# Kernel optimization log

Measured on AMD Instinct MI355X. Metric: run time of the kernel, lower is better.

The kernel has to match this reference:

```python
import jax, jax.numpy as jnp
import numpy as np

D_MODEL = 1024
NUM_HEADS = 16
HEAD_DIM = D_MODEL // NUM_HEADS
ROPE_BASE = 10000.0


def _rope_cos_sin(seq_len, head_dim, dtype):
    # inv_freq over half the head dim (standard 1D RoPE)
    inv_freq = 1.0 / (ROPE_BASE ** (jnp.arange(0, head_dim, 2, dtype=jnp.float32) / head_dim))
    ang = jnp.arange(seq_len, dtype=jnp.float32)[:, None] * inv_freq[None, :]  # [S, hd/2]
    cos = jnp.concatenate([jnp.cos(ang), jnp.cos(ang)], axis=-1).astype(dtype)  # [S, hd]
    sin = jnp.concatenate([jnp.sin(ang), jnp.sin(ang)], axis=-1).astype(dtype)
    return cos, sin


def _rotate_half(t):
    t1, t2 = jnp.split(t, 2, axis=-1)
    return jnp.concatenate([-t2, t1], axis=-1)


def _apply_rope(t, cos, sin):
    # t: [B, H, S, hd]; cos/sin: [S, hd]
    return t * cos[None, None, :, :] + _rotate_half(t) * sin[None, None, :, :]


def setup_inputs() -> dict:
    key = jax.random.key(0)
    k1, k2, k3 = jax.random.split(key, 3)
    B, S = 2, 2048
    x = jax.random.normal(k1, (B, S, D_MODEL), dtype=jnp.float32)
    w_qkv = jax.random.normal(k2, (D_MODEL, 3 * D_MODEL), dtype=jnp.float32) * (D_MODEL ** -0.5)
    w_proj = jax.random.normal(k3, (D_MODEL, D_MODEL), dtype=jnp.float32) * (D_MODEL ** -0.5)
    b_proj = jnp.zeros((D_MODEL,), dtype=jnp.float32)
    return {"x": x, "w_qkv": w_qkv, "w_proj": w_proj, "b_proj": b_proj, "causal": 1}


def reference(x, w_qkv, w_proj, b_proj, causal):
    B, S, D = x.shape
    scale = HEAD_DIM ** -0.5
    qkv = x @ w_qkv  # [B, S, 3D]
    q, k, v = jnp.split(qkv, 3, axis=-1)

    def to_heads(t):
        return t.reshape(B, S, NUM_HEADS, HEAD_DIM).transpose(0, 2, 1, 3)  # [B,H,S,hd]

    q, k, v = to_heads(q), to_heads(k), to_heads(v)

    cos, sin = _rope_cos_sin(S, HEAD_DIM, x.dtype)
    q = _apply_rope(q, cos, sin)
    k = _apply_rope(k, cos, sin)

    attn = jnp.einsum('bhqd,bhkd->bhqk', q, k) * scale  # [B,H,S,S]
    if causal:
        causal_mask = jnp.triu(jnp.ones((S, S), dtype=bool), k=1)
        attn = jnp.where(causal_mask[None, None, :, :], jnp.float32(-jnp.inf).astype(attn.dtype), attn)
    attn = jax.nn.softmax(attn, axis=-1)
    out = jnp.einsum('bhqk,bhkd->bhqd', attn, v)  # [B,H,S,hd]
    out = out.transpose(0, 2, 1, 3).reshape(B, S, D)
    return out @ w_proj + b_proj
```

## Files before the change

### kernel.cpp

```cpp
#include <hip/hip_runtime.h>
#include <stdint.h>
#include <math.h>

#define B_   2
#define S_   2048
#define D_   1024
#define H_   16
#define HD_  64
#define M_   (B_*S_)
#define N3_  (3*D_)

typedef __bf16 bf16;
typedef __bf16 bf16x2 __attribute__((ext_vector_type(2)));
typedef __bf16 bf16x4v __attribute__((ext_vector_type(4)));
typedef __bf16 bf16x8 __attribute__((ext_vector_type(8)));
typedef float  f32x4 __attribute__((ext_vector_type(4)));
typedef float  f32x16 __attribute__((ext_vector_type(16)));

__device__ __forceinline__ void gload_lds16(const void* g, void* l) {
  __builtin_amdgcn_global_load_lds(
      (__attribute__((address_space(1))) const unsigned int*)g,
      (__attribute__((address_space(3))) unsigned int*)l, 16, 0, 0);
}

__device__ __forceinline__ float fast_exp2(float x) {
  return __builtin_amdgcn_exp2f(x);
}

__global__ __launch_bounds__(256) void prep_kernel(const float* __restrict__ x, bf16* __restrict__ xb,
                                                   const float* __restrict__ w_qkv, bf16* __restrict__ wqkvT,
                                                   const float* __restrict__ w_proj, bf16* __restrict__ wprojT,
                                                   float* __restrict__ cosT, float* __restrict__ sinT) {
  __shared__ float tile[32][33];
  int blk = blockIdx.x, tid = threadIdx.x;
  if (blk < 1024) {
#pragma unroll
    for (int it = 0; it < 4; it++) {
      int i = (blk * 4 + it) * 256 + tid;
      float4 v = ((const float4*)x)[i];
      bf16x4v o;
      o[0] = (bf16)v.x; o[1] = (bf16)v.y; o[2] = (bf16)v.z; o[3] = (bf16)v.w;
      *(bf16x4v*)(xb + (size_t)i * 4) = o;
    }
  } else if (blk < 5120) {
    const float* in; bf16* out; int R, C, tb;
    if (blk < 4096) { in = w_qkv;  out = wqkvT;  R = 1024; C = 3072; tb = blk - 1024; }
    else            { in = w_proj; out = wprojT; R = 1024; C = 1024; tb = blk - 4096; }
    int nbx = C >> 5;
    int bx = tb % nbx, by = tb / nbx;
    int c0 = bx * 32, r0 = by * 32;
    int tx = tid & 31, ty = tid >> 5;
#pragma unroll
    for (int j = 0; j < 4; j++)
      tile[ty + j * 8][tx] = in[(size_t)(r0 + ty + j * 8) * C + c0 + tx];
    __syncthreads();
#pragma unroll
    for (int j = 0; j < 4; j++)
      out[(size_t)(c0 + ty + j * 8) * R + r0 + tx] = (bf16)tile[tx][ty + j * 8];
  } else {
    int i = (blk - 5120) * 256 + tid;
    int s = i >> 5, d = i & 31;
    float inv = powf(10000.0f, -(float)d * (1.0f / 32.0f));
    float a = (float)s * inv;
    float sv, cv;
    sincosf(a, &sv, &cv);
    cosT[i] = cv; sinT[i] = sv;
  }
}

__global__ __launch_bounds__(512, 4) void gemm_qkv(const bf16* __restrict__ A,
                                                   const bf16* __restrict__ Bt,
                                                   bf16* __restrict__ Cb,
                                                   const float* __restrict__ cosT,
                                                   const float* __restrict__ sinT,
                                                   bf16* __restrict__ vt) {
  __shared__ __align__(16) unsigned char lds[81920];
  const int K = 1024;
  int tid = threadIdx.x, lane = tid & 63, w = tid >> 6;
  int bid = blockIdx.y * gridDim.x + blockIdx.x;
  int sw = (bid & 7) * 64 + (bid >> 3);
  int bx = sw & 15, by = sw >> 4;
  int m0 = by * 128, n0 = bx * 192;
  int rl = lane & 15, kg = lane >> 4;

  int r8 = tid >> 3;
  int cSw = ((tid & 7) ^ (r8 & 7)) * 16;
  const char* Ab = (const char*)A;
  const char* Bb = (const char*)Bt;

#define QSTG(kt, bf)                                                                        \
  do {                                                                                      \
    char* base = (char*)lds + (bf) * 40960;                                                 \
    _Pragma("unroll")                                                                       \
    for (int s = 0; s < 2; s++)                                                             \
      gload_lds16(Ab + ((size_t)(m0 + s * 64 + r8) * K + (kt) * 64) * 2 + cSw,              \
                  base + s * 8192 + tid * 16);                                              \
    _Pragma("unroll")                                                                       \
    for (int s = 0; s < 3; s++)                                                             \
      gload_lds16(Bb + ((size_t)(n0 + s * 64 + r8) * K + (kt) * 64) * 2 + cSw,              \
                  base + 16384 + s * 8192 + tid * 16);                                      \
  } while (0)

  int ch0 = ((kg + 0) ^ (rl & 7)) * 16;
  int ch1 = ((kg + 4) ^ (rl & 7)) * 16;
  int aoff = (w * 16 + rl) * 128;

  f32x4 acc[12] = {};

  QSTG(0, 0);
  asm volatile("s_waitcnt vmcnt(0)" ::: "memory");
  __builtin_amdgcn_s_barrier();

  for (int kt = 0; kt < 16; kt++) {
    int cur = kt & 1;
    if (kt + 1 < 16) QSTG(kt + 1, cur ^ 1);
    const char* base = (const char*)lds + cur * 40960;
    bf16x8 a0 = *(const bf16x8*)(base + aoff + ch0);
    bf16x8 a1 = *(const bf16x8*)(base + aoff + ch1);
    __builtin_amdgcn_s_setprio(1);
#pragma unroll
    for (int br = 0; br < 12; br++) {
      int boff = 16384 + (br * 16 + rl) * 128;
      bf16x8 b0 = *(const bf16x8*)(base + boff + ch0);
      bf16x8 b1 = *(const bf16x8*)(base + boff + ch1);
      acc[br] = __builtin_amdgcn_mfma_f32_16x16x32_bf16(a0, b0, acc[br], 0, 0, 0);
      acc[br] = __builtin_amdgcn_mfma_f32_16x16x32_bf16(a1, b1, acc[br], 0, 0, 0);
    }
    __builtin_amdgcn_s_setprio(0);
    asm volatile("s_waitcnt vmcnt(0)" ::: "memory");
    __builtin_amdgcn_s_barrier();
  }

  int rq = kg * 4;
#pragma unroll
  for (int hb = 0; hb < 3; hb++) {
    int g0 = n0 + hb * 64;
    if (g0 < 2048) {
#pragma unroll
      for (int j = 0; j < 2; j++) {
        int br = hb * 4 + j;
#pragma unroll
        for (int r = 0; r < 4; r++) {
          int row = m0 + w * 16 + rq + r;
          int srw = row & 2047;
          int d2 = j * 16 + rl;
          float c = cosT[srw * 32 + d2], sn = sinT[srw * 32 + d2];
          float x1 = acc[br][r], x2 = acc[br + 2][r];
          size_t o = (size_t)row * 3072 + g0 + d2;
          Cb[o]      = (bf16)(x1 * c - x2 * sn);
          Cb[o + 32] = (bf16)(x2 * c + x1 * sn);
        }
      }
    } else {
      int posbase = ((rq & 4) << 1) | ((rq & 8) >> 1);
      int row0 = m0 + w * 16;
      int bb = row0 >> 11;
      int sbase = (row0 & 2047) + posbase;
#pragma unroll
      for (int j = 0; j < 4; j++) {
        int br = hb * 4 + j;
        int col = g0 + j * 16 + rl - 2048;
        bf16x4v pv;
        pv[0] = (bf16)acc[br][0]; pv[1] = (bf16)acc[br][1];
        pv[2] = (bf16)acc[br][2]; pv[3] = (bf16)acc[br][3];
        *(bf16x4v*)(vt + ((size_t)(bb * 1024 + col)) * 2048 + sbase) = pv;
      }
    }
  }
#undef QSTG
}

__global__ __launch_bounds__(256) void gemm_proj(const bf16* __restrict__ A,
                                                 const bf16* __restrict__ Bt,
                                                 float* __restrict__ Cf,
                                                 const float* __restrict__ bias) {
  __shared__ __align__(16) unsigned char As[8192];
  __shared__ __align__(16) unsigned char Bs[16384];
  const int K = 1024, N = 1024;
  int tid = threadIdx.x;
  int lane = tid & 63, w = tid >> 6;
  int bid = blockIdx.y * gridDim.x + blockIdx.x;
  int sw = (bid & 7) * 64 + (bid >> 3);
  int bx = sw & 7, by = sw >> 3;
  int m0 = by * 64, n0 = bx * 128;
  int m_off = (w >> 1) * 32, n_off = (w & 1) * 64;
  int rl = lane & 15, kg = lane >> 4;
  f32x4 acc[2][4] = {};

  const char* Ab = (const char*)A;
  const char* Bb = (const char*)Bt;
  int r8 = tid >> 3;
  int cSw = ((tid & 7) ^ (r8 & 7)) * 16;

  int ch0 = ((0 + kg) ^ (rl & 7)) * 16;
  int ch1 = ((4 + kg) ^ (rl & 7)) * 16;

  for (int k0 = 0; k0 < K; k0 += 64) {
#pragma unroll
    for (int s = 0; s < 2; s++) {
      int row = s * 32 + r8;
      gload_lds16(Ab + ((size_t)(m0 + row) * K + k0) * 2 + cSw, (char*)As + s * 4096 + tid * 16);
    }
#pragma unroll
    for (int s = 0; s < 4; s++) {
      int row = s * 32 + r8;
      gload_lds16(Bb + ((size_t)(n0 + row) * K + k0) * 2 + cSw, (char*)Bs + s * 4096 + tid * 16);
    }
    __syncthreads();
    bf16x8 a[2][2], b[4][2];
#pragma unroll
    for (int i = 0; i < 2; i++) {
      int row = m_off + i * 16 + rl;
      a[i][0] = *(const bf16x8*)((const char*)As + row * 128 + ch0);
      a[i][1] = *(const bf16x8*)((const char*)As + row * 128 + ch1);
    }
#pragma unroll
    for (int j = 0; j < 4; j++) {
      int row = n_off + j * 16 + rl;
      b[j][0] = *(const bf16x8*)((const char*)Bs + row * 128 + ch0);
      b[j][1] = *(const bf16x8*)((const char*)Bs + row * 128 + ch1);
    }
    __builtin_amdgcn_s_setprio(1);
#pragma unroll
    for (int i = 0; i < 2; i++)
#pragma unroll
      for (int j = 0; j < 4; j++) {
        acc[i][j] = __builtin_amdgcn_mfma_f32_16x16x32_bf16(a[i][0], b[j][0], acc[i][j], 0, 0, 0);
        acc[i][j] = __builtin_amdgcn_mfma_f32_16x16x32_bf16(a[i][1], b[j][1], acc[i][j], 0, 0, 0);
      }
    __builtin_amdgcn_s_setprio(0);
    __syncthreads();
  }

  int rq = kg * 4;
  for (int i = 0; i < 2; i++)
    for (int j = 0; j < 4; j++) {
      int col = n0 + n_off + j * 16 + rl;
      float bv = bias[col];
      for (int r = 0; r < 4; r++) {
        int row = m0 + m_off + i * 16 + rq + r;
        Cf[(size_t)row * N + col] = acc[i][j][r] + bv;
      }
    }
}

__global__ __launch_bounds__(512, 4) void attn_kernel(const bf16* __restrict__ qkv,
                                                      const bf16* __restrict__ vt,
                                                      bf16* __restrict__ O) {
  __shared__ __align__(16) unsigned char Ks[2][16384];
  __shared__ __align__(16) unsigned char Vs[2][16384];
  int tid = threadIdx.x, lane = tid & 63, w = tid >> 6;
  int qw = w & 3, p = w >> 2;
  int bid = blockIdx.x;
  int xcd = bid & 7, slot = bid >> 3;
  int bh = xcd * 4 + (slot & 3);
  int u = slot >> 2;
  int qt = 15 - u;
  int b = bh >> 4, h = bh & 15;
  int q0w = qt * 128 + qw * 32;
  int l31 = lane & 31, hi = lane >> 5;
  const char* qb = (const char*)qkv;
  const char* vb = (const char*)vt;

  int kr0 = tid >> 3, kcs = (tid & 7) ^ (kr0 & 7);
  int vr0 = tid >> 4, vcs = (tid & 15) ^ (vr0 & 7);

#define STAGE(buf, kvbase)                                                                              \
  do {                                                                                                  \
    gload_lds16(qb + (((size_t)(b * 2048 + (kvbase) + kr0) * 3072) + 1024 + h * 64) * 2 + kcs * 16,     \
                (char*)Ks[buf] + tid * 16);                                                             \
    gload_lds16(qb + (((size_t)(b * 2048 + (kvbase) + kr0 + 64) * 3072) + 1024 + h * 64) * 2 + kcs * 16,\
                (char*)Ks[buf] + (tid + 512) * 16);                                                     \
    gload_lds16(vb + (((size_t)(bh * 64 + vr0) * 2048) + (kvbase)) * 2 + vcs * 16,                      \
                (char*)Vs[buf] + tid * 16);                                                             \
    gload_lds16(vb + (((size_t)(bh * 64 + vr0 + 32) * 2048) + (kvbase)) * 2 + vcs * 16,                 \
                (char*)Vs[buf] + (tid + 512) * 16);                                                     \
  } while (0)

  bf16x8 aq[4];
#pragma unroll
  for (int s = 0; s < 4; s++) {
    size_t row = (size_t)(b * 2048 + q0w + l31);
    bf16x8 v = *(const bf16x8*)(qb + (row * 3072 + h * 64 + s * 16 + hi * 8) * 2);
#pragma unroll
    for (int e = 0; e < 8; e++) v[e] = (bf16)((float)v[e] * 0.18033688f);
    aq[s] = v;
  }

  f32x16 o0 = {}, o1 = {};
  float mrun = -3e38f, lrun = 0.f;
  int npair = qt + 1;

  STAGE(0, 0);
  asm volatile("s_waitcnt vmcnt(0)" ::: "memory");
  __builtin_amdgcn_s_barrier();

  for (int i = 0; i < npair; i++) {
    int cur = i & 1;
    if (i + 1 < npair) STAGE(cur ^ 1, (i + 1) * 128);

    int kvw = i * 128 + p * 64;
    if (kvw <= q0w + 31) {
      bool diag = (kvw + 63 > q0w);

      f32x16 scr[2];
#pragma unroll
      for (int kf = 0; kf < 2; kf++)
#pragma unroll
        for (int r = 0; r < 16; r++) scr[kf][r] = 0.f;
      __builtin_amdgcn_s_setprio(1);
#pragma unroll
      for (int s = 0; s < 4; s++) {
#pragma unroll
        for (int kf = 0; kf < 2; kf++) {
          int row = p * 64 + kf * 32 + l31;
          int ch = (hi + 2 * s) ^ (row & 7);
          bf16x8 ak = *(const bf16x8*)(Ks[cur] + row * 128 + ch * 16);
          scr[kf] = __builtin_amdgcn_mfma_f32_32x32x16_bf16(ak, aq[s], scr[kf], 0, 0, 0);
        }
      }
      __builtin_amdgcn_s_setprio(0);

      int qg = q0w + l31;
      if (diag) {
#pragma unroll
        for (int kf = 0; kf < 2; kf++)
#pragma unroll
          for (int r = 0; r < 16; r++) {
            int k = kvw + kf * 32 + (r & 3) + 8 * (r >> 2) + 4 * hi;
            if (k > qg) scr[kf][r] = -3e38f;
          }
      }

      float mx = -3e38f;
#pragma unroll
      for (int kf = 0; kf < 2; kf++)
#pragma unroll
        for (int r = 0; r < 16; r++) mx = fmaxf(mx, scr[kf][r]);
      mx = fmaxf(mx, __shfl_xor(mx, 32));

      if (!__all(mx - mrun <= 11.5f)) {
        float mnew = fmaxf(mrun, mx);
        float corr = exp2f(mrun - mnew);
        mrun = mnew;
        lrun *= corr;
#pragma unroll
        for (int r = 0; r < 16; r++) {
          float cr = __shfl(corr, (r & 3) + 8 * (r >> 2) + 4 * hi);
          o0[r] *= cr; o1[r] *= cr;
        }
      }

      float rs = 0.f;
      unsigned D[2][8];
#pragma unroll
      for (int kf = 0; kf < 2; kf++)
#pragma unroll
        for (int j = 0; j < 8; j++) {
          float p0 = fast_exp2(scr[kf][2 * j] - mrun);
          float p1 = fast_exp2(scr[kf][2 * j + 1] - mrun);
          rs += p0 + p1;
          bf16x2 tp; tp[0] = (bf16)p0; tp[1] = (bf16)p1;
          D[kf][j] = __builtin_bit_cast(unsigned, tp);
        }
      rs += __shfl_xor(rs, 32);
      lrun += rs;

#pragma unroll
      for (int kf = 0; kf < 2; kf++) {
#pragma unroll
        for (int sg = 0; sg < 2; sg++) {
          union { unsigned u4[4]; bf16x8 v; } ap;
          ap.u4[0] = D[kf][4 * sg + 0];
          ap.u4[1] = D[kf][4 * sg + 1];
          ap.u4[2] = D[kf][4 * sg + 2];
          ap.u4[3] = D[kf][4 * sg + 3];
          __builtin_amdgcn_s_setprio(1);
#pragma unroll
          for (int nf = 0; nf < 2; nf++) {
            int row = nf * 32 + l31;
            int ch = ((p * 8) + (hi + 2 * sg + 4 * kf)) ^ (row & 7);
            bf16x8 bv = *(const bf16x8*)(Vs[cur] + row * 256 + ch * 16);
            if (nf == 0) o0 = __builtin_amdgcn_mfma_f32_32x32x16_bf16(ap.v, bv, o0, 0, 0, 0);
            else         o1 = __builtin_amdgcn_mfma_f32_32x32x16_bf16(ap.v, bv, o1, 0, 0, 0);
          }
          __builtin_amdgcn_s_setprio(0);
        }
      }
    }

    asm volatile("s_waitcnt vmcnt(0)" ::: "memory");
    __builtin_amdgcn_s_barrier();
  }

  float* mlb = (float*)Ks;
  if (hi == 0) {
    mlb[((qw * 2 + p) * 2 + 0) * 32 + l31] = mrun;
    mlb[((qw * 2 + p) * 2 + 1) * 32 + l31] = lrun;
  }
  __syncthreads();
  float m_o = mlb[((qw * 2 + (1 - p)) * 2 + 0) * 32 + l31];
  float l_o = mlb[((qw * 2 + (1 - p)) * 2 + 1) * 32 + l31];
  float Mm = fmaxf(mrun, m_o);
  float cs = exp2f(mrun - Mm);
  float L  = lrun * cs + l_o * exp2f(m_o - Mm);
  float* obuf = (float*)Vs;
  if (p == 1) {
#pragma unroll
    for (int r = 0; r < 16; r++) {
      int crow = (r & 3) + 8 * (r >> 2) + 4 * hi;
      float c = __shfl(cs, crow);
      obuf[qw * 2048 + r * 64 + lane]        = o0[r] * c;
      obuf[qw * 2048 + (r + 16) * 64 + lane] = o1[r] * c;
    }
  }
  __syncthreads();
  if (p == 0) {
    float linv = 1.0f / L;
#pragma unroll
    for (int r = 0; r < 16; r++) {
      int crow = (r & 3) + 8 * (r >> 2) + 4 * hi;
      float c  = __shfl(cs, crow);
      float li = __shfl(linv, crow);
      size_t row = (size_t)(b * 2048 + q0w + crow);
      float v0 = (o0[r] * c + obuf[qw * 2048 + r * 64 + lane]) * li;
      float v1 = (o1[r] * c + obuf[qw * 2048 + (r + 16) * 64 + lane]) * li;
      O[row * 1024 + h * 64 + l31]      = (bf16)v0;
      O[row * 1024 + h * 64 + 32 + l31] = (bf16)v1;
    }
  }
#undef STAGE
}

extern "C" void kernel_launch(void* const* d_in, const int* in_sizes, int n_in,
                              void* d_out, int out_size, void* d_ws, size_t ws_size,
                              hipStream_t stream) {
  const float* x      = (const float*)d_in[0];
  const float* w_qkv  = (const float*)d_in[1];
  const float* w_proj = (const float*)d_in[2];
  const float* b_proj = (const float*)d_in[3];

  char* ws = (char*)d_ws;
  size_t off = 0;
  bf16* xb     = (bf16*)(ws + off); off += (size_t)M_ * D_ * 2;
  bf16* wqkvT  = (bf16*)(ws + off); off += (size_t)N3_ * D_ * 2;
  bf16* wprojT = (bf16*)(ws + off); off += (size_t)D_ * D_ * 2;
  bf16* qkvb   = (bf16*)(ws + off); off += (size_t)M_ * N3_ * 2;
  bf16* ob     = (bf16*)(ws + off); off += (size_t)M_ * D_ * 2;
  bf16* vtb    = (bf16*)(ws + off); off += (size_t)M_ * D_ * 2;
  float* cosT  = (float*)(ws + off); off += (size_t)S_ * 32 * 4;
  float* sinT  = (float*)(ws + off); off += (size_t)S_ * 32 * 4;

  prep_kernel<<<5376, 256, 0, stream>>>(x, xb, w_qkv, wqkvT, w_proj, wprojT, cosT, sinT);
  gemm_qkv<<<dim3(16, 32), 512, 0, stream>>>(xb, wqkvT, qkvb, cosT, sinT, vtb);
  attn_kernel<<<512, 512, 0, stream>>>(qkvb, vtb, ob);
  gemm_proj<<<dim3(8, 64), 256, 0, stream>>>(ob, wprojT, (float*)d_out, b_proj);
}
```

Measured before the change: 96.77 us.

## Split attention into 64-row query tiles with 4-way KV split per tile

Each attention block now covers 64 query rows (2 query waves) instead of 128, and splits each 256-key chunk across 4 KV-parallel wave groups. The launch doubles to 1024 blocks. Double-buffered async K/V staging is replaced by a single 64KB buffer loaded and waited on synchronously each iteration. The final merge now combines four partial softmax states through LDS. The aim is finer-grained work and better balance across the causal triangle, at the cost of losing load/compute overlap, halving occupancy via launch bounds, and wasting more work on masked tiles.

```diff
diff --git a/kernel.cpp b/kernel.cpp
--- a/kernel.cpp
+++ b/kernel.cpp
@@ -244,38 +244,26 @@
     }
 }
 
-__global__ __launch_bounds__(512, 4) void attn_kernel(const bf16* __restrict__ qkv,
+__global__ __launch_bounds__(512, 2) void attn_kernel(const bf16* __restrict__ qkv,
                                                       const bf16* __restrict__ vt,
                                                       bf16* __restrict__ O) {
-  __shared__ __align__(16) unsigned char Ks[2][16384];
-  __shared__ __align__(16) unsigned char Vs[2][16384];
+  __shared__ __align__(16) unsigned char smem[65536];
   int tid = threadIdx.x, lane = tid & 63, w = tid >> 6;
-  int qw = w & 3, p = w >> 2;
+  int qw = w & 1, p = w >> 1;
   int bid = blockIdx.x;
-  int xcd = bid & 7, slot = bid >> 3;
-  int bh = xcd * 4 + (slot & 3);
-  int u = slot >> 2;
-  int qt = 15 - u;
+  int u = bid >> 5;
+  int t64 = 31 - u;
+  int jb = bid & 31;
+  int bh = (jb & 7) * 4 + (jb >> 3);
   int b = bh >> 4, h = bh & 15;
-  int q0w = qt * 128 + qw * 32;
+  int q0w = t64 * 64 + qw * 32;
   int l31 = lane & 31, hi = lane >> 5;
   const char* qb = (const char*)qkv;
   const char* vb = (const char*)vt;
 
-  int kr0 = tid >> 3, kcs = (tid & 7) ^ (kr0 & 7);
-  int vr0 = tid >> 4, vcs = (tid & 15) ^ (vr0 & 7);
-
-#define STAGE(buf, kvbase)                                                                              \
-  do {                                                                                                  \
-    gload_lds16(qb + (((size_t)(b * 2048 + (kvbase) + kr0) * 3072) + 1024 + h * 64) * 2 + kcs * 16,     \
-                (char*)Ks[buf] + tid * 16);                                                             \
-    gload_lds16(qb + (((size_t)(b * 2048 + (kvbase) + kr0 + 64) * 3072) + 1024 + h * 64) * 2 + kcs * 16,\
-                (char*)Ks[buf] + (tid + 512) * 16);                                                     \
-    gload_lds16(vb + (((size_t)(bh * 64 + vr0) * 2048) + (kvbase)) * 2 + vcs * 16,                      \
-                (char*)Vs[buf] + tid * 16);                                                             \
-    gload_lds16(vb + (((size_t)(bh * 64 + vr0 + 32) * 2048) + (kvbase)) * 2 + vcs * 16,                 \
-                (char*)Vs[buf] + (tid + 512) * 16);                                                     \
-  } while (0)
+  int l3 = lane >> 3;
+  int kcS = ((lane & 7) ^ (l3 & 7)) * 16;
+  int d5 = lane >> 5;
 
   bf16x8 aq[4];
 #pragma unroll
@@ -289,17 +277,27 @@
 
   f32x16 o0 = {}, o1 = {};
   float mrun = -3e38f, lrun = 0.f;
-  int npair = qt + 1;
-
-  STAGE(0, 0);
-  asm volatile("s_waitcnt vmcnt(0)" ::: "memory");
-  __builtin_amdgcn_s_barrier();
+  int npair = t64 / 4 + 1;
 
   for (int i = 0; i < npair; i++) {
-    int cur = i & 1;
-    if (i + 1 < npair) STAGE(cur ^ 1, (i + 1) * 128);
-
-    int kvw = i * 128 + p * 64;
+    int kv0 = i * 256;
+#pragma unroll
+    for (int s = 0; s < 4; s++) {
+      int row = s * 64 + w * 8 + l3;
+      gload_lds16(qb + (((size_t)(b * 2048 + kv0 + row) * 3072) + 1024 + h * 64) * 2 + kcS,
+                  (char*)smem + (s * 64 + w * 8) * 128 + lane * 16);
+    }
+#pragma unroll
+    for (int s = 0; s < 4; s++) {
+      int d = s * 16 + w * 2 + d5;
+      int vch = ((lane & 31) ^ (d & 7)) * 16;
+      gload_lds16(vb + (((size_t)(bh * 64 + d) * 2048) + kv0) * 2 + vch,
+                  (char*)smem + 32768 + (s * 16 + w * 2) * 512 + lane * 16);
+    }
+    asm volatile("s_waitcnt vmcnt(0)" ::: "memory");
+    __builtin_amdgcn_s_barrier();
+
+    int kvw = kv0 + p * 64;
     if (kvw <= q0w + 31) {
       bool diag = (kvw + 63 > q0w);
 
@@ -314,8 +312,8 @@
 #pragma unroll
         for (int kf = 0; kf < 2; kf++) {
           int row = p * 64 + kf * 32 + l31;
-          int ch = (hi + 2 * s) ^ (row & 7);
-          bf16x8 ak = *(const bf16x8*)(Ks[cur] + row * 128 + ch * 16);
+          int ch = (hi + 2 * s) ^ (l31 & 7);
+          bf16x8 ak = *(const bf16x8*)((const char*)smem + row * 128 + ch * 16);
           scr[kf] = __builtin_amdgcn_mfma_f32_32x32x16_bf16(ak, aq[s], scr[kf], 0, 0, 0);
         }
       }
@@ -378,9 +376,9 @@
           __builtin_amdgcn_s_setprio(1);
 #pragma unroll
           for (int nf = 0; nf < 2; nf++) {
-            int row = nf * 32 + l31;
-            int ch = ((p * 8) + (hi + 2 * sg + 4 * kf)) ^ (row & 7);
-            bf16x8 bv = *(const bf16x8*)(Vs[cur] + row * 256 + ch * 16);
+            int d = nf * 32 + l31;
+            int ch = p * 8 + ((hi + 2 * sg + 4 * kf) ^ (d & 7));
+            bf16x8 bv = *(const bf16x8*)((const char*)smem + 32768 + d * 512 + ch * 16);
             if (nf == 0) o0 = __builtin_amdgcn_mfma_f32_32x32x16_bf16(ap.v, bv, o0, 0, 0, 0);
             else         o1 = __builtin_amdgcn_mfma_f32_32x32x16_bf16(ap.v, bv, o1, 0, 0, 0);
           }
@@ -388,48 +386,56 @@
         }
       }
     }
-
-    asm volatile("s_waitcnt vmcnt(0)" ::: "memory");
     __builtin_amdgcn_s_barrier();
   }
 
-  float* mlb = (float*)Ks;
+  float* mlb  = (float*)(smem + 63488);
+  float* obuf = (float*)smem;
   if (hi == 0) {
-    mlb[((qw * 2 + p) * 2 + 0) * 32 + l31] = mrun;
-    mlb[((qw * 2 + p) * 2 + 1) * 32 + l31] = lrun;
+    mlb[(qw * 4 + p) * 64 + l31]      = mrun;
+    mlb[(qw * 4 + p) * 64 + 32 + l31] = lrun;
   }
   __syncthreads();
-  float m_o = mlb[((qw * 2 + (1 - p)) * 2 + 0) * 32 + l31];
-  float l_o = mlb[((qw * 2 + (1 - p)) * 2 + 1) * 32 + l31];
-  float Mm = fmaxf(mrun, m_o);
-  float cs = exp2f(mrun - Mm);
-  float L  = lrun * cs + l_o * exp2f(m_o - Mm);
-  float* obuf = (float*)Vs;
-  if (p == 1) {
+  float mj[4], lj[4];
+#pragma unroll
+  for (int j = 0; j < 4; j++) {
+    mj[j] = mlb[(qw * 4 + j) * 64 + l31];
+    lj[j] = mlb[(qw * 4 + j) * 64 + 32 + l31];
+  }
+  float M = fmaxf(fmaxf(mj[0], mj[1]), fmaxf(mj[2], mj[3]));
+  float L = lj[0] * exp2f(mj[0] - M) + lj[1] * exp2f(mj[1] - M)
+          + lj[2] * exp2f(mj[2] - M) + lj[3] * exp2f(mj[3] - M);
+  float Smine = exp2f(mrun - M);
+  float Li = 1.0f / L;
+  if (p != 0) {
+    int slot = qw * 3 + (p - 1);
 #pragma unroll
     for (int r = 0; r < 16; r++) {
       int crow = (r & 3) + 8 * (r >> 2) + 4 * hi;
-      float c = __shfl(cs, crow);
-      obuf[qw * 2048 + r * 64 + lane]        = o0[r] * c;
-      obuf[qw * 2048 + (r + 16) * 64 + lane] = o1[r] * c;
+      float sc = __shfl(Smine, crow);
+      obuf[slot * 2048 + crow * 64 + l31]      = o0[r] * sc;
+      obuf[slot * 2048 + crow * 64 + 32 + l31] = o1[r] * sc;
     }
   }
   __syncthreads();
   if (p == 0) {
-    float linv = 1.0f / L;
 #pragma unroll
     for (int r = 0; r < 16; r++) {
       int crow = (r & 3) + 8 * (r >> 2) + 4 * hi;
-      float c  = __shfl(cs, crow);
-      float li = __shfl(linv, crow);
+      float sc = __shfl(Smine, crow);
+      float li = __shfl(Li, crow);
+      float v0 = o0[r] * sc, v1 = o1[r] * sc;
+#pragma unroll
+      for (int j = 0; j < 3; j++) {
+        int slot = qw * 3 + j;
+        v0 += obuf[slot * 2048 + crow * 64 + l31];
+        v1 += obuf[slot * 2048 + crow * 64 + 32 + l31];
+      }
       size_t row = (size_t)(b * 2048 + q0w + crow);
-      float v0 = (o0[r] * c + obuf[qw * 2048 + r * 64 + lane]) * li;
-      float v1 = (o1[r] * c + obuf[qw * 2048 + (r + 16) * 64 + lane]) * li;
-      O[row * 1024 + h * 64 + l31]      = (bf16)v0;
-      O[row * 1024 + h * 64 + 32 + l31] = (bf16)v1;
-    }
-  }
-#undef STAGE
+      O[row * 1024 + h * 64 + l31]      = (bf16)(v0 * li);
+      O[row * 1024 + h * 64 + 32 + l31] = (bf16)(v1 * li);
+    }
+  }
 }
 
 extern "C" void kernel_launch(void* const* d_in, const int* in_sizes, int n_in,
@@ -453,6 +459,6 @@
 
   prep_kernel<<<5376, 256, 0, stream>>>(x, xb, w_qkv, wqkvT, w_proj, wprojT, cosT, sinT);
   gemm_qkv<<<dim3(16, 32), 512, 0, stream>>>(xb, wqkvT, qkvb, cosT, sinT, vtb);
-  attn_kernel<<<512, 512, 0, stream>>>(qkvb, vtb, ob);
+  attn_kernel<<<1024, 512, 0, stream>>>(qkvb, vtb, ob);
   gemm_proj<<<dim3(8, 64), 256, 0, stream>>>(ob, wprojT, (float*)d_out, b_proj);
 }
```

After: 109.1 us. 12.7% more time.
